# Kernel optimization log

Hardware: AMD Instinct MI355X
Metric: run time of the kernel (lower is better)

Reference implementation:

```python
import jax, jax.numpy as jnp
import numpy as np

MAX_LEN, BATCH, D_IN, D_H = 512, 128, 512, 512


def setup_inputs() -> dict:
    key = jax.random.key(0)
    ks = jax.random.split(key, 9)
    s_in = 1.0 / np.sqrt(D_IN)
    s_h = 1.0 / np.sqrt(D_H)
    return {
        "seq": jax.random.normal(ks[0], (MAX_LEN, BATCH, D_IN), jnp.float32),
        "W_iz": jax.random.normal(ks[1], (D_H, D_IN), jnp.float32) * s_in,
        "b_iz": jax.random.normal(ks[2], (D_H,), jnp.float32) * s_in,
        "W_in": jax.random.normal(ks[3], (D_H, D_IN), jnp.float32) * s_in,
        "b_in": jax.random.normal(ks[4], (D_H,), jnp.float32) * s_in,
        "W_hz": jax.random.normal(ks[5], (D_H, D_H), jnp.float32) * s_h,
        "b_hz": jax.random.normal(ks[6], (D_H,), jnp.float32) * s_h,
        "W_hn": jax.random.normal(ks[7], (D_H, D_H), jnp.float32) * s_h,
        "b_hn": jax.random.normal(ks[8], (D_H,), jnp.float32) * s_h,
    }


def reference(seq, W_iz, b_iz, W_in, b_in, W_hz, b_hz, W_hn, b_hn):
    # Precompute input projections for all timesteps in one big GEMM each.
    # iz, inn: [max_len, batch, hidden]
    iz = jnp.einsum("tbi,hi->tbh", seq, W_iz) + b_iz
    inn = jnp.einsum("tbi,hi->tbh", seq, W_in) + b_in
    h0 = jnp.zeros((seq.shape[1], W_hz.shape[0]), seq.dtype)

    def step(h_prev, xs):
        iz_t, in_t = xs
        z_t = jax.nn.sigmoid(iz_t + h_prev @ W_hz.T + b_hz)
        # NOTE: original module sets r_t = ones, so no reset gating.
        n_t = jnp.tanh(in_t + (h_prev @ W_hn.T + b_hn))
        h_t = (1.0 - z_t) * n_t + z_t * h_prev
        return h_t, h_t

    _, H = jax.lax.scan(step, h0, (iz, inn))  # H: [max_len, batch, hidden]
    return H[None]  # [1, max_len, batch, hidden] (H.unsqueeze(0))
```

## Files before the change

### kernel.cpp

```cpp
#include <hip/hip_runtime.h>
#include <stdint.h>

typedef _Float16 f16x8 __attribute__((ext_vector_type(8)));
typedef _Float16 f16x4 __attribute__((ext_vector_type(4)));
typedef float    f32x4 __attribute__((ext_vector_type(4)));
typedef unsigned int u32x4v __attribute__((ext_vector_type(4)));

#define T_LEN 512
#define RLX   __ATOMIC_RELAXED
#define AGT   __HIP_MEMORY_SCOPE_AGENT

union PK4 { _Float16 h[4]; unsigned long long q; };
union QZ  { unsigned long long q; f16x4 v; };

__device__ __forceinline__ void gload_lds16(const void* gsrc, void* ldsdst) {
    auto g = (const __attribute__((address_space(1))) void*)(reinterpret_cast<uintptr_t>(gsrc));
    auto s = (__attribute__((address_space(3))) void*)(reinterpret_cast<uintptr_t>(ldsdst));
    __builtin_amdgcn_global_load_lds(g, s, 16, 0, 0);
}

__global__ __launch_bounds__(256) void prep_misc(
    const float* __restrict__ W_iz, const float* __restrict__ W_in,
    const float* __restrict__ W_hz, const float* __restrict__ W_hn,
    const float* __restrict__ b_iz, const float* __restrict__ b_in,
    const float* __restrict__ b_hz, const float* __restrict__ b_hn,
    _Float16* __restrict__ Wci, _Float16* __restrict__ Whc,
    float* __restrict__ bc, unsigned int* __restrict__ hbuf32)
{
    const int tid = blockIdx.x * 256 + threadIdx.x;
    if (tid < 131072) {
        const bool is_h = tid >= 65536;
        const int u = tid & 65535;
        const int e = u * 8;
        const int row = e >> 9;
        const int k = e & 511;
        const float* s;
        if (!is_h) s = (row < 512) ? (W_iz + (size_t)row * 512 + k)
                                   : (W_in + (size_t)(row - 512) * 512 + k);
        else       s = (row < 512) ? (W_hz + (size_t)row * 512 + k)
                                   : (W_hn + (size_t)(row - 512) * 512 + k);
        f32x4 a = *(const f32x4*)s;
        f32x4 b = *(const f32x4*)(s + 4);
        f16x8 o;
        o[0] = (_Float16)a[0]; o[1] = (_Float16)a[1];
        o[2] = (_Float16)a[2]; o[3] = (_Float16)a[3];
        o[4] = (_Float16)b[0]; o[5] = (_Float16)b[1];
        o[6] = (_Float16)b[2]; o[7] = (_Float16)b[3];
        _Float16* d = is_h ? Whc : Wci;
        *(f16x8*)(d + e) = o;
    } else if (tid < 132096) {
        const int j2 = tid - 131072;
        bc[j2] = (j2 < 512) ? (b_iz[j2] + b_hz[j2]) : (b_in[j2 - 512] + b_hn[j2 - 512]);
    } else if (tid < 164864) {
        const int u = tid - 132096;
        u32x4v z = {0u, 0u, 0u, 0u};
        *(u32x4v*)(hbuf32 + (size_t)u * 4) = z;
    }
}

__global__ __launch_bounds__(256) void gemm_proj(
    const float* __restrict__ A,
    const _Float16* __restrict__ Bw,
    const float* __restrict__ bc,
    _Float16* Co)
{
    __shared__ _Float16 As[128 * 40];
    __shared__ _Float16 Bs[128 * 32];

    const int mt = blockIdx.x;
    const int nt = blockIdx.y;
    const int m0 = mt * 128, n0 = nt * 128;
    const int tid = threadIdx.x;
    const int w = tid >> 6, l = tid & 63;
    const int wr = w >> 1, wc = w & 1;
    const int lrow = l & 15, lk = l >> 4;

    f32x4 acc[4][4] = {};

    const int arow = tid >> 1;
    const int acol = (tid & 1) * 16;

    for (int kt = 0; kt < 16; ++kt) {
        const int k0 = kt * 32;
        if (kt) __syncthreads();
        const float* as = A + (size_t)(m0 + arow) * 512 + k0 + acol;
        f32x4 a0 = *(const f32x4*)as;
        f32x4 a1 = *(const f32x4*)(as + 4);
        f32x4 a2 = *(const f32x4*)(as + 8);
        f32x4 a3 = *(const f32x4*)(as + 12);
        f16x8 h0, h1;
#pragma unroll
        for (int e = 0; e < 4; ++e) {
            h0[e] = (_Float16)a0[e]; h0[4 + e] = (_Float16)a1[e];
            h1[e] = (_Float16)a2[e]; h1[4 + e] = (_Float16)a3[e];
        }
        *(f16x8*)&As[arow * 40 + acol] = h0;
        *(f16x8*)&As[arow * 40 + acol + 8] = h1;
#pragma unroll
        for (int i = 0; i < 2; ++i) {
            const int chunk = w * 2 + i;
            const _Float16* gsrc =
                Bw + (size_t)(n0 + chunk * 16 + (l >> 2)) * 512 + k0 + (l & 3) * 8;
            gload_lds16(gsrc, &Bs[chunk * 512]);
        }
        __syncthreads();
        f16x8 af[4], bf[4];
#pragma unroll
        for (int i = 0; i < 4; ++i) {
            af[i] = *(const f16x8*)&As[(wr * 64 + i * 16 + lrow) * 40 + lk * 8];
            bf[i] = *(const f16x8*)&Bs[(wc * 64 + i * 16 + lrow) * 32 + lk * 8];
        }
#pragma unroll
        for (int mi = 0; mi < 4; ++mi)
#pragma unroll
            for (int ni = 0; ni < 4; ++ni)
                acc[mi][ni] = __builtin_amdgcn_mfma_f32_16x16x32_f16(
                    bf[ni], af[mi], acc[mi][ni], 0, 0, 0);
    }
    const int gate = nt >> 2;
#pragma unroll
    for (int mi = 0; mi < 4; ++mi) {
#pragma unroll
        for (int p = 0; p < 2; ++p) {
            const int j2q0 = n0 + wc * 64 + p * 32 + 4 * lk;
            const f32x4 b0 = *(const f32x4*)&bc[j2q0];
            const f32x4 b1 = *(const f32x4*)&bc[j2q0 + 16];
            f16x8 o;
#pragma unroll
            for (int r = 0; r < 4; ++r) {
                o[r]     = (_Float16)(acc[mi][2 * p][r]     + b0[r]);
                o[4 + r] = (_Float16)(acc[mi][2 * p + 1][r] + b1[r]);
            }
            const int blk_s = (wr * 4 + mi) * 16 + (nt & 3) * 4 + wc * 2 + p;
            _Float16* dst = Co + ((((size_t)mt * 128 + blk_s) * 2 + gate) * 512) + l * 8;
            *(f16x8*)dst = o;
        }
    }
}

__global__ __launch_bounds__(512, 1) void gru_scan(
    const _Float16* __restrict__ Whc,
    const char* izb,
    float* Hout,
    unsigned int* hbuf32)
{
    __shared__ _Float16 hlds[2 * 16 * 512];

    const int blk  = blockIdx.x;
    const int g    = blk & 7;
    const int slot = blk >> 3;
    const int tid  = threadIdx.x;
    const int wv   = tid >> 6;
    const int l    = tid & 63;
    const int lrow = l & 15, lk = l >> 4;
    const int jbase = slot * 128 + wv * 16;
    const int jq    = jbase + 4 * lk;
    const int bg    = 16 * g + lrow;
    const int blk_s = 16 * g + 4 * slot + (wv >> 1);
    const int stage_b = tid >> 5;
    const int stage_jq = 4 * (tid & 31);

    f16x8 wz[16], wn[16];
#pragma unroll
    for (int s = 0; s < 16; ++s) {
        wz[s] = *(const f16x8*)&Whc[(size_t)(jbase + lrow) * 512 + s * 32 + lk * 8];
        wn[s] = *(const f16x8*)&Whc[(size_t)(512 + jbase + lrow) * 512 + s * 32 + lk * 8];
    }
#pragma unroll
    for (int s = 0; s < 16; ++s) {
        asm volatile("" : "+v"(wz[s]));
        asm volatile("" : "+v"(wn[s]));
    }

    *(unsigned long long*)&hlds[(lrow * 512 + jq) ^ ((lrow & 7) << 3)] = 0ull;

    QZ pz, pn, npz, npn;
    {
        const char* rec = izb + ((size_t)0 * 128 + blk_s) * 2048 + l * 16 + (wv & 1) * 8;
        pz.q = *(const unsigned long long*)rec;
        pn.q = *(const unsigned long long*)(rec + 1024);
    }

    float hm[4] = {0.f, 0.f, 0.f, 0.f};

    for (int t = 0; t < T_LEN; ++t) {
        const int par = (t + 1) & 1;
        const int lp  = t & 1;
        const unsigned long long tp =
            (unsigned long long)(unsigned)t | ((unsigned long long)(unsigned)t << 32);

        const unsigned long long* hb64 =
            (const unsigned long long*)(hbuf32 + (size_t)par * 65536);
        unsigned long long q0[3], q1[3];
        int pix[3];
#pragma unroll
        for (int i = 0; i < 3; ++i) {
            const int s_i = (slot + 1 + i) & 3;
            const int u32i = (16 * g + stage_b) * 512 + s_i * 128 + stage_jq;
            pix[i] = u32i >> 1;
            q0[i] = __hip_atomic_load(hb64 + pix[i],     RLX, AGT);
            q1[i] = __hip_atomic_load(hb64 + pix[i] + 1, RLX, AGT);
        }
        while (true) {
            unsigned long long x = 0;
#pragma unroll
            for (int i = 0; i < 3; ++i)
                x |= (q0[i] ^ tp) | (q1[i] ^ tp);
            if (__all((x & 0x0000FFFF0000FFFFull) == 0)) break;
#pragma unroll
            for (int i = 0; i < 3; ++i) {
                q0[i] = __hip_atomic_load(hb64 + pix[i],     RLX, AGT);
                q1[i] = __hip_atomic_load(hb64 + pix[i] + 1, RLX, AGT);
            }
        }

        if (t + 1 < T_LEN) {
            const char* rec = izb + ((size_t)(t + 1) * 128 + blk_s) * 2048
                              + l * 16 + (wv & 1) * 8;
            npz.q = *(const unsigned long long*)rec;
            npn.q = *(const unsigned long long*)(rec + 1024);
        }
        __builtin_amdgcn_sched_barrier(0);

#pragma unroll
        for (int i = 0; i < 3; ++i) {
            const int s_i = (slot + 1 + i) & 3;
            const unsigned int w0 = ((unsigned int)(q0[i] >> 16)) & 0xFFFFu;
            const unsigned int w1 = (unsigned int)(q0[i] >> 48);
            const unsigned int w2 = ((unsigned int)(q1[i] >> 16)) & 0xFFFFu;
            const unsigned int w3 = (unsigned int)(q1[i] >> 48);
            const unsigned long long out =
                (unsigned long long)(w0 | (w1 << 16)) |
                ((unsigned long long)(w2 | (w3 << 16)) << 32);
            const int idx = (lp * 8192 + stage_b * 512 + s_i * 128 + stage_jq)
                            ^ ((stage_b & 7) << 3);
            *(unsigned long long*)&hlds[idx] = out;
        }

        __syncthreads();

        f32x4 az = {0.f, 0.f, 0.f, 0.f}, an = {0.f, 0.f, 0.f, 0.f};
        const int hbase = lp * 8192 + lrow * 512;
        const int sw = (lrow & 7) << 3;
#pragma unroll
        for (int s = 0; s < 16; ++s) {
            const f16x8 hf = *(const f16x8*)&hlds[(hbase + s * 32 + lk * 8) ^ sw];
            az = __builtin_amdgcn_mfma_f32_16x16x32_f16(wz[s], hf, az, 0, 0, 0);
            an = __builtin_amdgcn_mfma_f32_16x16x32_f16(wn[s], hf, an, 0, 0, 0);
        }

        PK4 own;
        f32x4 Hv;
#pragma unroll
        for (int r = 0; r < 4; ++r) {
            float zpre = az[r] + (float)pz.v[r];
            float npre = an[r] + (float)pn.v[r];
            zpre = fminf(fmaxf(zpre, -30.f), 30.f);
            const float z = 1.f / (1.f + __expf(-zpre));
            npre = fminf(fmaxf(npre, -15.f), 15.f);
            const float e2 = __expf(2.f * npre);
            const float n = (e2 - 1.f) / (e2 + 1.f);
            hm[r] = (1.f - z) * n + z * hm[r];
            Hv[r] = hm[r];
            own.h[r] = (_Float16)hm[r];
        }

        *(unsigned long long*)
            &hlds[(((t + 1) & 1) * 8192 + lrow * 512 + jq) ^ ((lrow & 7) << 3)] = own.q;

        if (t < T_LEN - 1) {
            asm volatile("s_waitcnt vmcnt(0)" ::: "memory");
            __builtin_amdgcn_sched_barrier(0);
            const unsigned long long tagp =
                (unsigned long long)(unsigned)(t + 1) |
                ((unsigned long long)(unsigned)(t + 1) << 32);
            const unsigned long long d0 =
                ((own.q & 0xFFFFull) << 16) |
                (((own.q >> 16) & 0xFFFFull) << 48) | tagp;
            const unsigned long long d1 =
                (((own.q >> 32) & 0xFFFFull) << 16) |
                (((own.q >> 48) & 0xFFFFull) << 48) | tagp;
            unsigned long long* hw = (unsigned long long*)
                (hbuf32 + (size_t)(t & 1) * 65536 + (size_t)bg * 512 + jq);
            __hip_atomic_store(hw,     d0, RLX, AGT);
            __hip_atomic_store(hw + 1, d1, RLX, AGT);
        }

        *(f32x4*)&Hout[(size_t)t * 65536 + (size_t)bg * 512 + jq] = Hv;

        pz = npz; pn = npn;
    }
}

extern "C" void kernel_launch(void* const* d_in, const int* in_sizes, int n_in,
                              void* d_out, int out_size, void* d_ws, size_t ws_size,
                              hipStream_t stream) {
    (void)in_sizes; (void)n_in; (void)out_size; (void)ws_size;
    const float* seq  = (const float*)d_in[0];
    const float* W_iz = (const float*)d_in[1];
    const float* b_iz = (const float*)d_in[2];
    const float* W_in = (const float*)d_in[3];
    const float* b_in = (const float*)d_in[4];
    const float* W_hz = (const float*)d_in[5];
    const float* b_hz = (const float*)d_in[6];
    const float* W_hn = (const float*)d_in[7];
    const float* b_hn = (const float*)d_in[8];

    char* ws = (char*)d_ws;
    _Float16*     Wci    = (_Float16*)(ws);
    _Float16*     Whc    = (_Float16*)(ws + 1048576);
    float*        bc     = (float*)   (ws + 2097152);
    unsigned int* hbuf32 = (unsigned int*)(ws + 2101248);

    prep_misc<<<644, 256, 0, stream>>>(W_iz, W_in, W_hz, W_hn,
                                       b_iz, b_in, b_hz, b_hn,
                                       Wci, Whc, bc, hbuf32);
    gemm_proj<<<dim3(512, 8), 256, 0, stream>>>(seq, Wci, bc, (_Float16*)d_out);
    gru_scan<<<32, 512, 0, stream>>>(Whc, (const char*)d_out, (float*)d_out, hbuf32);
}
```

Before: 1.915 ms.

## Prefetch input projections two steps ahead with double-buffered registers

```diff
diff --git a/kernel.cpp b/kernel.cpp
--- a/kernel.cpp
+++ b/kernel.cpp
@@ -166,31 +166,30 @@
         wz[s] = *(const f16x8*)&Whc[(size_t)(jbase + lrow) * 512 + s * 32 + lk * 8];
         wn[s] = *(const f16x8*)&Whc[(size_t)(512 + jbase + lrow) * 512 + s * 32 + lk * 8];
     }
-#pragma unroll
-    for (int s = 0; s < 16; ++s) {
-        asm volatile("" : "+v"(wz[s]));
-        asm volatile("" : "+v"(wn[s]));
-    }
 
     *(unsigned long long*)&hlds[(lrow * 512 + jq) ^ ((lrow & 7) << 3)] = 0ull;
 
-    QZ pz, pn, npz, npn;
+    QZ ez, en, oz, on;
     {
-        const char* rec = izb + ((size_t)0 * 128 + blk_s) * 2048 + l * 16 + (wv & 1) * 8;
-        pz.q = *(const unsigned long long*)rec;
-        pn.q = *(const unsigned long long*)(rec + 1024);
+        const char* r0 = izb + ((size_t)0 * 128 + blk_s) * 2048 + l * 16 + (wv & 1) * 8;
+        ez.q = *(const unsigned long long*)r0;
+        en.q = *(const unsigned long long*)(r0 + 1024);
+        const char* r1 = izb + ((size_t)1 * 128 + blk_s) * 2048 + l * 16 + (wv & 1) * 8;
+        oz.q = *(const unsigned long long*)r1;
+        on.q = *(const unsigned long long*)(r1 + 1024);
     }
 
     float hm[4] = {0.f, 0.f, 0.f, 0.f};
 
-    for (int t = 0; t < T_LEN; ++t) {
+    const unsigned long long* hb64base = (const unsigned long long*)hbuf32;
+
+    auto step = [&](int t, QZ& cz, QZ& cn) {
         const int par = (t + 1) & 1;
         const int lp  = t & 1;
         const unsigned long long tp =
             (unsigned long long)(unsigned)t | ((unsigned long long)(unsigned)t << 32);
 
-        const unsigned long long* hb64 =
-            (const unsigned long long*)(hbuf32 + (size_t)par * 65536);
+        const unsigned long long* hb64 = hb64base + (size_t)par * 32768;
         unsigned long long q0[3], q1[3];
         int pix[3];
 #pragma unroll
@@ -213,14 +212,6 @@
                 q1[i] = __hip_atomic_load(hb64 + pix[i] + 1, RLX, AGT);
             }
         }
-
-        if (t + 1 < T_LEN) {
-            const char* rec = izb + ((size_t)(t + 1) * 128 + blk_s) * 2048
-                              + l * 16 + (wv & 1) * 8;
-            npz.q = *(const unsigned long long*)rec;
-            npn.q = *(const unsigned long long*)(rec + 1024);
-        }
-        __builtin_amdgcn_sched_barrier(0);
 
 #pragma unroll
         for (int i = 0; i < 3; ++i) {
@@ -244,6 +235,7 @@
         const int sw = (lrow & 7) << 3;
 #pragma unroll
         for (int s = 0; s < 16; ++s) {
+            asm volatile("" : "+v"(wz[s]), "+v"(wn[s]));
             const f16x8 hf = *(const f16x8*)&hlds[(hbase + s * 32 + lk * 8) ^ sw];
             az = __builtin_amdgcn_mfma_f32_16x16x32_f16(wz[s], hf, az, 0, 0, 0);
             an = __builtin_amdgcn_mfma_f32_16x16x32_f16(wn[s], hf, an, 0, 0, 0);
@@ -253,8 +245,8 @@
         f32x4 Hv;
 #pragma unroll
         for (int r = 0; r < 4; ++r) {
-            float zpre = az[r] + (float)pz.v[r];
-            float npre = an[r] + (float)pn.v[r];
+            float zpre = az[r] + (float)cz.v[r];
+            float npre = an[r] + (float)cn.v[r];
             zpre = fminf(fmaxf(zpre, -30.f), 30.f);
             const float z = 1.f / (1.f + __expf(-zpre));
             npre = fminf(fmaxf(npre, -15.f), 15.f);
@@ -265,11 +257,23 @@
             own.h[r] = (_Float16)hm[r];
         }
 
+        if (t + 2 < T_LEN) {
+            const char* rec = izb + ((size_t)(t + 2) * 128 + blk_s) * 2048
+                              + l * 16 + (wv & 1) * 8;
+            cz.q = *(const unsigned long long*)rec;
+            cn.q = *(const unsigned long long*)(rec + 1024);
+        }
+        __builtin_amdgcn_sched_barrier(0);
+
         *(unsigned long long*)
             &hlds[(((t + 1) & 1) * 8192 + lrow * 512 + jq) ^ ((lrow & 7) << 3)] = own.q;
 
         if (t < T_LEN - 1) {
-            asm volatile("s_waitcnt vmcnt(0)" ::: "memory");
+            if (t + 2 < T_LEN) {
+                asm volatile("s_waitcnt vmcnt(2)" ::: "memory");
+            } else {
+                asm volatile("s_waitcnt vmcnt(0)" ::: "memory");
+            }
             __builtin_amdgcn_sched_barrier(0);
             const unsigned long long tagp =
                 (unsigned long long)(unsigned)(t + 1) |
@@ -287,8 +291,11 @@
         }
 
         *(f32x4*)&Hout[(size_t)t * 65536 + (size_t)bg * 512 + jq] = Hv;
-
-        pz = npz; pn = npn;
+    };
+
+    for (int t = 0; t < T_LEN; t += 2) {
+        step(t,     ez, en);
+        step(t + 1, oz, on);
     }
 }
 
```

Result: faster. 1.827 ms (-4.6%).
